# Kernel tuning notes

Hardware: AMD Instinct MI355X
Metric: run time of the kernel (lower is better)

The kernel has to match this reference:

```python
import jax, jax.numpy as jnp
import numpy as np
import math


def l2norm(x, axis):
    n = jnp.linalg.norm(x, axis=axis, keepdims=True)
    return x / jnp.maximum(n, 1e-12)


def token_pooling(x, w1, b1, w2, b2, p, w3, b3, w4, b4, eps=1e-6):
    # x: [B, L, dim_in]
    h = jnp.maximum(x @ w1 + b1, 0.0) @ w2 + b2        # [B, L, 512]
    h = l2norm(h, -1)
    # GeM over token dim L (avg_pool1d over full length == mean)
    g = jnp.mean(jnp.clip(h, eps, None) ** p, axis=1) ** (1.0 / p)  # [B, 512]
    o = jnp.maximum(g @ w3 + b3, 0.0) @ w4 + b4        # [B, dim_out]
    return l2norm(o, -1)


def sinkhorn_log(S_aug, log_a, log_b, num_iters=3):
    # S_aug: [B, m+1, n]; reg = 1.0
    M = S_aug
    u = jnp.zeros_like(log_a)
    v = jnp.zeros_like(log_b)
    def body(carry, _):
        u, v = carry
        u = log_a - jax.nn.logsumexp(M + v[:, None, :], axis=2)
        v = log_b - jax.nn.logsumexp(M + u[:, :, None], axis=1)
        return (u, v), None
    (u, v), _ = jax.lax.scan(body, (u, v), None, length=num_iters)
    return M + u[:, :, None] + v[:, None, :]


def setup_inputs() -> dict:
    key = jax.random.key(0)
    ks = jax.random.split(key, 16)
    B, S, N, C = 4, 4, 1029, 2048
    def w(k, shape):
        return jax.random.normal(k, shape, dtype=jnp.float32) * 0.02
    inp = {
        "tokens": jax.random.normal(ks[0], (B, S, N, C), dtype=jnp.float32),
        "patch_start_idx": 5,
        # camera token pooling
        "cam_w1": w(ks[1], (2048, 1024)), "cam_b1": jnp.zeros((1024,), jnp.float32),
        "cam_w2": w(ks[2], (1024, 512)),  "cam_b2": jnp.zeros((512,), jnp.float32),
        "cam_p":  jnp.ones((1,), jnp.float32) * 3.0,
        "cam_w3": w(ks[3], (512, 512)),   "cam_b3": jnp.zeros((512,), jnp.float32),
        "cam_w4": w(ks[4], (512, 256)),   "cam_b4": jnp.zeros((256,), jnp.float32),
        # register token pooling
        "reg_w1": w(ks[5], (2048, 1024)), "reg_b1": jnp.zeros((1024,), jnp.float32),
        "reg_w2": w(ks[6], (1024, 512)),  "reg_b2": jnp.zeros((512,), jnp.float32),
        "reg_p":  jnp.ones((1,), jnp.float32) * 3.0,
        "reg_w3": w(ks[7], (512, 512)),   "reg_b3": jnp.zeros((512,), jnp.float32),
        "reg_w4": w(ks[8], (512, 256)),   "reg_b4": jnp.zeros((256,), jnp.float32),
        # patch cluster features (1x1 convs == linear over channel dim)
        "pf_w1": w(ks[9], (2048, 512)),   "pf_b1": jnp.zeros((512,), jnp.float32),
        "pf_w2": w(ks[10], (512, 128)),   "pf_b2": jnp.zeros((128,), jnp.float32),
        # patch scores
        "ps_w1": w(ks[11], (2048, 512)),  "ps_b1": jnp.zeros((512,), jnp.float32),
        "ps_w2": w(ks[12], (512, 64)),    "ps_b2": jnp.zeros((64,), jnp.float32),
        "dust_bin": jnp.array(1.0, jnp.float32),
    }
    return inp


def reference(tokens, patch_start_idx, cam_w1, cam_b1, cam_w2, cam_b2, cam_p, cam_w3, cam_b3, cam_w4, cam_b4, reg_w1, reg_b1, reg_w2, reg_b2, reg_p, reg_w3, reg_b3, reg_w4, reg_b4, pf_w1, pf_b1, pf_w2, pf_b2, ps_w1, ps_b1, ps_w2, ps_b2, dust_bin):
    B, S, N, C = tokens.shape
    psi = int(patch_start_idx)
    # camera token: [B, S, C]
    camera = token_pooling(tokens[:, :, 0], cam_w1, cam_b1, cam_w2, cam_b2, cam_p, cam_w3, cam_b3, cam_w4, cam_b4)
    # register tokens: [B, S*(psi-1), C]
    reg_tok = tokens[:, :, 1:psi].reshape(B, S * (psi - 1), C)
    register = token_pooling(reg_tok, reg_w1, reg_b1, reg_w2, reg_b2, reg_p, reg_w3, reg_b3, reg_w4, reg_b4)
    # patch tokens flattened over (S, Np): n = S*Np
    patch = tokens[:, :, psi:].reshape(B, -1, C)              # [B, n, C]
    n = patch.shape[1]
    feats = jnp.maximum(patch @ pf_w1 + pf_b1, 0.0) @ pf_w2 + pf_b2   # [B, n, 128]
    scores = jnp.maximum(patch @ ps_w1 + ps_b1, 0.0) @ ps_w2 + ps_b2  # [B, n, 64]
    S_mat = jnp.swapaxes(scores, 1, 2)                        # [B, m, n]
    m = S_mat.shape[1]
    # augment with dustbin row
    dust_row = jnp.broadcast_to(dust_bin, (B, 1, n)).astype(S_mat.dtype)
    S_aug = jnp.concatenate([S_mat, dust_row], axis=1)        # [B, m+1, n]
    norm = -math.log(n + m)
    log_a = jnp.full((m + 1,), norm, dtype=S_mat.dtype).at[-1].add(math.log(n - m))
    log_b = jnp.full((n,), norm, dtype=S_mat.dtype)
    log_a = jnp.broadcast_to(log_a, (B, m + 1))
    log_b = jnp.broadcast_to(log_b, (B, n))
    log_P = sinkhorn_log(S_aug, log_a, log_b, num_iters=3) - norm
    p = jnp.exp(log_P)[:, :-1, :]                             # [B, m, n]
    # (f * p).sum(-1) as batched matmul: [B, cluster_dim, m]
    pooled = jnp.einsum('bnc,bkn->bck', feats, p)
    patch_result = l2norm(pooled, 1).reshape(B, -1)           # [B, cluster_dim*m]
    return jnp.concatenate([patch_result, camera, register], axis=-1)
```

## Files before the change

kernel.cpp:

```cpp
#include <hip/hip_runtime.h>

typedef unsigned short u16;
typedef unsigned int u32;

#define B_ 4
#define S_ 4
#define NTOK 1029
#define CDIM 2048
#define PSI 5
#define NPB 4096
#define MROWS 16384
#define N1 1024
#define N2 256
#define MD 64
#define MA 65

using bf16x8 = __attribute__((ext_vector_type(8))) short;
using f32x4  = __attribute__((ext_vector_type(4))) float;
using u16x8  = __attribute__((ext_vector_type(8))) unsigned short;

typedef __attribute__((address_space(1))) const void global_cvoid;
typedef __attribute__((address_space(3))) void lds_void;

__device__ __forceinline__ u16 f2b(float f) {
  u32 u = __builtin_bit_cast(u32, f);
  u32 r = (u + 0x7fffu + ((u >> 16) & 1u)) >> 16;
  return (u16)r;
}

__global__ void k_convert_patch(const float* __restrict__ tokens, u16* __restrict__ Abf) {
  size_t idx = (size_t)blockIdx.x * 256 + threadIdx.x;
  size_t r = idx >> 8;
  int cv = (int)(idx & 255) << 3;
  int b = (int)(r >> 12), s = (int)((r >> 10) & 3), j = (int)(r & 1023);
  const float* src = tokens + ((size_t)((b * S_ + s) * NTOK + PSI + j)) * CDIM + cv;
  float4 v0 = *(const float4*)src;
  float4 v1 = *(const float4*)(src + 4);
  u16x8 o;
  o[0] = f2b(v0.x); o[1] = f2b(v0.y); o[2] = f2b(v0.z); o[3] = f2b(v0.w);
  o[4] = f2b(v1.x); o[5] = f2b(v1.y); o[6] = f2b(v1.z); o[7] = f2b(v1.w);
  *(u16x8*)(Abf + r * CDIM + cv) = o;
}

__global__ void k_pack_patch(const float* __restrict__ pfw1, const float* __restrict__ psw1,
                             const float* __restrict__ pfw2, const float* __restrict__ psw2,
                             const float* __restrict__ pfb1, const float* __restrict__ psb1,
                             const float* __restrict__ pfb2, const float* __restrict__ psb2,
                             u16* __restrict__ W1t, u16* __restrict__ W2t,
                             float* __restrict__ b1c, float* __restrict__ b2c) {
  __shared__ float tile[32][33];
  int id = blockIdx.x, tid = threadIdx.x;
  int tx = tid & 31, ty = tid >> 5;
  if (id < 2048) {
    int kb = (id & 63) * 32, nb = (id >> 6) * 32;
    #pragma unroll
    for (int i = 0; i < 4; ++i) {
      int k = kb + ty + i * 8, n = nb + tx;
      tile[ty + i * 8][tx] = (n < 512) ? pfw1[(size_t)k * 512 + n] : psw1[(size_t)k * 512 + (n - 512)];
    }
    __syncthreads();
    #pragma unroll
    for (int i = 0; i < 4; ++i) {
      int n = nb + ty + i * 8, k = kb + tx;
      W1t[(size_t)n * CDIM + k] = f2b(tile[tx][ty + i * 8]);
    }
  } else if (id < 2304) {
    int i2 = id - 2048;
    int kb = (i2 & 31) * 32, jb = (i2 >> 5) * 32;
    #pragma unroll
    for (int i = 0; i < 4; ++i) {
      int k = kb + ty + i * 8, j = jb + tx;
      float v = 0.f;
      if (j < 128) { if (k < 512) v = pfw2[(size_t)k * 128 + j]; }
      else if (j < 192) { if (k >= 512) v = psw2[(size_t)(k - 512) * 64 + (j - 128)]; }
      tile[ty + i * 8][tx] = v;
    }
    __syncthreads();
    #pragma unroll
    for (int i = 0; i < 4; ++i) {
      int j = jb + ty + i * 8, k = kb + tx;
      W2t[(size_t)j * N1 + k] = f2b(tile[tx][ty + i * 8]);
    }
  } else {
    int t = (id - 2304) * 256 + tid;
    if (t < 1024) b1c[t] = (t < 512) ? pfb1[t] : psb1[t - 512];
    if (t < 256)  b2c[t] = (t < 128) ? pfb2[t] : ((t < 192) ? psb2[t - 128] : 0.f);
  }
}

__global__ void k_pack_cr(const float* __restrict__ camw1, const float* __restrict__ regw1,
                          const float* __restrict__ camw2, const float* __restrict__ regw2,
                          const float* __restrict__ tokens,
                          u16* __restrict__ Bt1cr, u16* __restrict__ Bt2cr,
                          u16* __restrict__ Acr) {
  __shared__ float tile[32][33];
  int id = blockIdx.x, tid = threadIdx.x;
  int tx = tid & 31, ty = tid >> 5;
  if (id < 4096) {
    const float* src = (id < 2048) ? camw1 : regw1;
    u16* dst = Bt1cr + ((id < 2048) ? 0 : (size_t)1024 * CDIM);
    int i2 = id & 2047;
    int kb = (i2 & 63) * 32, nb = (i2 >> 6) * 32;
    #pragma unroll
    for (int i = 0; i < 4; ++i)
      tile[ty + i * 8][tx] = src[(size_t)(kb + ty + i * 8) * 1024 + nb + tx];
    __syncthreads();
    #pragma unroll
    for (int i = 0; i < 4; ++i)
      dst[(size_t)(nb + ty + i * 8) * CDIM + kb + tx] = f2b(tile[tx][ty + i * 8]);
  } else if (id < 5120) {
    int i3 = id - 4096;
    const float* src = (i3 < 512) ? camw2 : regw2;
    u16* dst = Bt2cr + ((i3 < 512) ? 0 : (size_t)512 * N1);
    int i2 = i3 & 511;
    int kb = (i2 & 31) * 32, nb = (i2 >> 5) * 32;
    #pragma unroll
    for (int i = 0; i < 4; ++i)
      tile[ty + i * 8][tx] = src[(size_t)(kb + ty + i * 8) * 512 + nb + tx];
    __syncthreads();
    #pragma unroll
    for (int i = 0; i < 4; ++i)
      dst[(size_t)(nb + ty + i * 8) * N1 + kb + tx] = f2b(tile[tx][ty + i * 8]);
  } else {
    int r = id - 5120;
    int c0 = tid << 3;
    u16x8 o;
    if (r >= 80) {
      #pragma unroll
      for (int i = 0; i < 8; ++i) o[i] = 0;
    } else {
      const float* src;
      if (r < 16) { int b = r >> 2, s = r & 3; src = tokens + ((size_t)(b * S_ + s) * NTOK) * CDIM; }
      else { int r2 = r - 16; int b = r2 >> 4, q = r2 & 15, s = q >> 2, t = (q & 3) + 1;
             src = tokens + ((size_t)(b * S_ + s) * NTOK + t) * CDIM; }
      float4 v0 = *(const float4*)(src + c0);
      float4 v1 = *(const float4*)(src + c0 + 4);
      o[0] = f2b(v0.x); o[1] = f2b(v0.y); o[2] = f2b(v0.z); o[3] = f2b(v0.w);
      o[4] = f2b(v1.x); o[5] = f2b(v1.y); o[6] = f2b(v1.z); o[7] = f2b(v1.w);
    }
    *(u16x8*)(Acr + (size_t)r * CDIM + c0) = o;
  }
}

#define STAGE_TILE(buf, k0)                                                    \
  {                                                                            \
    _Pragma("unroll")                                                          \
    for (int r = 0; r < 4; ++r) {                                              \
      __builtin_amdgcn_global_load_lds(                                        \
          (global_cvoid*)(A + abase + (size_t)(r * 32) * K + (k0)),            \
          (lds_void*)(&As[buf][lofs + r * 2048]), 16, 0, 0);                   \
      __builtin_amdgcn_global_load_lds(                                        \
          (global_cvoid*)(Bt + bbase + (size_t)(r * 32) * K + (k0)),           \
          (lds_void*)(&Bs[buf][lofs + r * 2048]), 16, 0, 0);                   \
    }                                                                          \
  }

#define COMPUTE_TILE(buf)                                                      \
  {                                                                            \
    _Pragma("unroll")                                                          \
    for (int kk = 0; kk < 64; kk += 32) {                                      \
      const int csw = (kk + hi8) ^ ((lane & 7) << 3);                          \
      bf16x8 af[4], bfr[4];                                                    \
      _Pragma("unroll")                                                        \
      for (int i = 0; i < 4; ++i) {                                            \
        af[i]  = *(const bf16x8*)&As[buf][((wr << 6) + (i << 4) + (lane & 15)) * 64 + csw]; \
        bfr[i] = *(const bf16x8*)&Bs[buf][((wc << 6) + (i << 4) + (lane & 15)) * 64 + csw]; \
      }                                                                        \
      _Pragma("unroll")                                                        \
      for (int mi = 0; mi < 4; ++mi)                                           \
        _Pragma("unroll")                                                      \
        for (int ni = 0; ni < 4; ++ni)                                         \
          acc[mi][ni] = __builtin_amdgcn_mfma_f32_16x16x32_bf16(af[mi], bfr[ni], acc[mi][ni], 0, 0, 0); \
    }                                                                          \
  }

template <int RELU, int OUTBF>
__global__ __launch_bounds__(256, 2)
void k_gemm(const u16* __restrict__ A, const u16* __restrict__ Bt,
            const float* __restrict__ bias, void* __restrict__ Cout,
            int M, int N, int K) {
  __shared__ u16 As[2][128 * 64];
  __shared__ u16 Bs[2][128 * 64];
  const int tid = threadIdx.x;
  const int lane = tid & 63;
  const int wave = tid >> 6;
  const int tM = blockIdx.x << 7;
  const int tN = blockIdx.y << 7;
  const int wr = wave >> 1, wc = wave & 1;
  const int hi8 = (lane >> 4) << 3;

  const int srow = (wave << 3) + (lane >> 3);
  const int scolsw = ((lane & 7) ^ (lane >> 3)) << 3;
  const size_t abase = (size_t)(tM + srow) * K + scolsw;
  const size_t bbase = (size_t)(tN + srow) * K + scolsw;
  const int lofs = (wave << 9) + (lane << 3);

  f32x4 acc[4][4];
  #pragma unroll
  for (int i = 0; i < 4; ++i)
    #pragma unroll
    for (int j = 0; j < 4; ++j)
      acc[i][j] = (f32x4){0.f, 0.f, 0.f, 0.f};

  const int nt = K >> 6;
  STAGE_TILE(0, 0)
  STAGE_TILE(1, 64)
  for (int t = 0; t < nt; t += 2) {
    asm volatile("s_waitcnt vmcnt(8)" ::: "memory");
    __builtin_amdgcn_s_barrier();
    COMPUTE_TILE(0)
    __builtin_amdgcn_s_barrier();
    if (t + 2 < nt) STAGE_TILE(0, (t + 2) << 6)
    if (t + 1 == nt - 1) {
      asm volatile("s_waitcnt vmcnt(0)" ::: "memory");
    } else {
      asm volatile("s_waitcnt vmcnt(8)" ::: "memory");
    }
    __builtin_amdgcn_s_barrier();
    COMPUTE_TILE(1)
    __builtin_amdgcn_s_barrier();
    if (t + 3 < nt) STAGE_TILE(1, (t + 3) << 6)
  }

  #pragma unroll
  for (int ni = 0; ni < 4; ++ni) {
    const int col = tN + (wc << 6) + (ni << 4) + (lane & 15);
    const float bv = bias[col];
    #pragma unroll
    for (int mi = 0; mi < 4; ++mi) {
      #pragma unroll
      for (int j = 0; j < 4; ++j) {
        const int row = tM + (wr << 6) + (mi << 4) + ((lane >> 4) << 2) + j;
        float vv = acc[mi][ni][j] + bv;
        if (RELU) vv = fmaxf(vv, 0.f);
        if (OUTBF) ((u16*)Cout)[(size_t)row * N + col] = f2b(vv);
        else       ((float*)Cout)[(size_t)row * N + col] = vv;
      }
    }
  }
}

__global__ __launch_bounds__(256, 2)
void k_gemm_splitk(const u16* __restrict__ A, const u16* __restrict__ Bt,
                   float* __restrict__ part, int N, int K, int KC) {
  __shared__ u16 As1[128 * 64];
  __shared__ u16 Bs1[128 * 64];
  const int tid = threadIdx.x;
  const int lane = tid & 63;
  const int wave = tid >> 6;
  const int tN = blockIdx.y << 7;
  const int kb = blockIdx.z * KC;
  const int wr = wave >> 1, wc = wave & 1;
  const int srow = (wave << 3) + (lane >> 3);
  const int scol = (lane & 7) << 3;
  const size_t abase = (size_t)srow * K + scol;
  const size_t bbase = (size_t)(tN + srow) * K + scol;
  u16* asw = &As1[(wave << 9) + (lane << 3)];
  u16* bsw = &Bs1[(wave << 9) + (lane << 3)];

  f32x4 acc[4][4];
  #pragma unroll
  for (int i = 0; i < 4; ++i)
    #pragma unroll
    for (int j = 0; j < 4; ++j)
      acc[i][j] = (f32x4){0.f, 0.f, 0.f, 0.f};

  for (int k0 = kb; k0 < kb + KC; k0 += 64) {
    #pragma unroll
    for (int r = 0; r < 4; ++r) {
      __builtin_amdgcn_global_load_lds(
          (global_cvoid*)(A + abase + (size_t)(r * 32) * K + k0),
          (lds_void*)(asw + r * 2048), 16, 0, 0);
      __builtin_amdgcn_global_load_lds(
          (global_cvoid*)(Bt + bbase + (size_t)(r * 32) * K + k0),
          (lds_void*)(bsw + r * 2048), 16, 0, 0);
    }
    __syncthreads();
    #pragma unroll
    for (int kk = 0; kk < 64; kk += 32) {
      bf16x8 af[4], bfr[4];
      #pragma unroll
      for (int i = 0; i < 4; ++i) {
        af[i]  = *(const bf16x8*)&As1[((wr << 6) + (i << 4) + (lane & 15)) * 64 + kk + ((lane >> 4) << 3)];
        bfr[i] = *(const bf16x8*)&Bs1[((wc << 6) + (i << 4) + (lane & 15)) * 64 + kk + ((lane >> 4) << 3)];
      }
      #pragma unroll
      for (int mi = 0; mi < 4; ++mi)
        #pragma unroll
        for (int ni = 0; ni < 4; ++ni)
// ... 94 lines not shown
  const float* w = W3 + (size_t)(kq << 7) * 512 + o;
  #pragma unroll 8
  for (int kk = 0; kk < 128; ++kk) acc += gls[(kq << 7) + kk] * w[(size_t)kk * 512];
  part[kq][col] = acc;
  __syncthreads();
  if (kq == 0) {
    float s = part[0][col] + part[1][col] + part[2][col] + part[3][col] + B3[o];
    o1b[pb * 512 + o] = fmaxf(s, 0.f);
  }
}

__global__ __launch_bounds__(512)
void k_cr3c(const float* __restrict__ o1b,
            const float* __restrict__ camw4, const float* __restrict__ regw4,
            const float* __restrict__ camb4, const float* __restrict__ regb4,
            float* __restrict__ out) {
  __shared__ float o1s[512];
  __shared__ float part[2][256];
  __shared__ float vsq[256];
  __shared__ float red[4];
  int pb = blockIdx.x;
  bool cam = (pb < 4);
  int path = pb >> 2, b = pb & 3;
  const float* W4 = cam ? camw4 : regw4;
  const float* B4 = cam ? camb4 : regb4;
  int tid = threadIdx.x;
  o1s[tid] = o1b[pb * 512 + tid];
  __syncthreads();
  int col = tid & 255, kh = tid >> 8;
  float acc = 0.f;
  const float* w = W4 + (size_t)(kh << 8) * 256 + col;
  #pragma unroll 8
  for (int kk = 0; kk < 256; ++kk) acc += o1s[(kh << 8) + kk] * w[(size_t)kk * 256];
  part[kh][col] = acc;
  __syncthreads();
  float val = 0.f;
  if (kh == 0) {
    val = part[0][col] + part[1][col] + B4[col];
    vsq[col] = val * val;
  }
  __syncthreads();
  float ss = (tid < 256) ? vsq[tid] : 0.f;
  #pragma unroll
  for (int o = 32; o; o >>= 1) ss += __shfl_down(ss, o);
  if (tid < 256 && (tid & 63) == 0) red[tid >> 6] = ss;
  __syncthreads();
  if (kh == 0) {
    float tot = red[0] + red[1] + red[2] + red[3];
    float inv = 1.f / fmaxf(sqrtf(tot), 1e-12f);
    out[(size_t)b * 8704 + 8192 + path * 256 + col] = val * inv;
  }
}

__global__ void k_tr_scores(const float* __restrict__ FS, const float* __restrict__ dust,
                            float* __restrict__ Sc) {
  __shared__ float t[64][65];
  int b = blockIdx.x >> 6, n0 = (blockIdx.x & 63) * 64;
  int tx = threadIdx.x & 63, ty = threadIdx.x >> 6;
  for (int r = ty; r < 64; r += 4)
    t[r][tx] = FS[((size_t)(b * NPB + n0 + r)) * N2 + 128 + tx];
  __syncthreads();
  for (int k = ty; k < 64; k += 4)
    Sc[((size_t)(b * MA) + k) * NPB + n0 + tx] = t[tx][k];
  if (threadIdx.x < 64)
    Sc[((size_t)(b * MA) + 64) * NPB + n0 + threadIdx.x] = dust[0];
}

__global__ void k_sink_u(const float* __restrict__ Sc, const float* __restrict__ v,
                         float* __restrict__ u) {
  __shared__ float redm[4], reds[4];
  int b = blockIdx.x / MA, k = blockIdx.x % MA;
  const float* row = Sc + ((size_t)(b * MA) + k) * NPB;
  const float* vb = v + (size_t)b * NPB;
  int tid = threadIdx.x;
  float mx = -1e30f, s = 0.f;
  for (int n = tid; n < NPB; n += 256) {
    float x = row[n] + vb[n];
    float m2 = fmaxf(mx, x);
    s = s * __expf(mx - m2) + __expf(x - m2);
    mx = m2;
  }
  #pragma unroll
  for (int o = 32; o; o >>= 1) {
    float mo = __shfl_down(mx, o), so = __shfl_down(s, o);
    float m2 = fmaxf(mx, mo);
    s = s * __expf(mx - m2) + so * __expf(mo - m2);
    mx = m2;
  }
  if ((tid & 63) == 0) { redm[tid >> 6] = mx; reds[tid >> 6] = s; }
  __syncthreads();
  if (tid == 0) {
    float M = redm[0];
    #pragma unroll
    for (int i = 1; i < 4; ++i) M = fmaxf(M, redm[i]);
    float S = 0.f;
    #pragma unroll
    for (int i = 0; i < 4; ++i) S += reds[i] * __expf(redm[i] - M);
    const float nrm = -logf((float)(NPB + MD));
    float la = (k == MD) ? (nrm + logf((float)(NPB - MD))) : nrm;
    u[b * MA + k] = la - (M + __logf(S));
  }
}

__global__ void k_sink_v(const float* __restrict__ Sc, const float* __restrict__ u,
                         float* __restrict__ v) {
  __shared__ float us[MA];
  int b = blockIdx.x >> 4;
  int n = ((blockIdx.x & 15) << 8) + threadIdx.x;
  if (threadIdx.x < MA) us[threadIdx.x] = u[b * MA + threadIdx.x];
  __syncthreads();
  const float* Sb = Sc + (size_t)b * MA * NPB + n;
  float mx = -1e30f;
  for (int k = 0; k < MA; ++k) mx = fmaxf(mx, Sb[(size_t)k * NPB] + us[k]);
  float s = 0.f;
  for (int k = 0; k < MA; ++k) s += __expf(Sb[(size_t)k * NPB] + us[k] - mx);
  const float nrm = -logf((float)(NPB + MD));
  v[(size_t)b * NPB + n] = nrm - (mx + __logf(s));
}

__global__ __launch_bounds__(256)
void k_pooled1(const float* __restrict__ FS, const float* __restrict__ Sc,
               const float* __restrict__ u, const float* __restrict__ v,
               float* __restrict__ partial) {
  __shared__ float Fs[64][132];
  __shared__ float Ps[64][68];
  int b = blockIdx.x >> 6, j = blockIdx.x & 63;
  int n0 = j << 6;
  int tid = threadIdx.x;
  {
    int r = tid >> 5;
    int c4 = (tid & 31) << 2;
    #pragma unroll
    for (int i = 0; i < 8; ++i) {
      int n = r + (i << 3);
      float4 vv = *(const float4*)&FS[((size_t)(b * NPB + n0 + n)) * N2 + c4];
      *(float4*)&Fs[n][c4] = vv;
    }
  }
  {
    const float nrm = -logf((float)(NPB + MD));
    int r = tid >> 4;
    int c4 = (tid & 15) << 2;
    #pragma unroll
    for (int i = 0; i < 4; ++i) {
      int k = r + (i << 4);
      float uk = u[b * MA + k];
      float4 sv = *(const float4*)&Sc[((size_t)(b * MA) + k) * NPB + n0 + c4];
      float4 vv = *(const float4*)&v[(size_t)b * NPB + n0 + c4];
      float4 o;
      o.x = __expf(sv.x + uk + vv.x - nrm);
      o.y = __expf(sv.y + uk + vv.y - nrm);
      o.z = __expf(sv.z + uk + vv.z - nrm);
      o.w = __expf(sv.w + uk + vv.w - nrm);
      *(float4*)&Ps[k][c4] = o;
    }
  }
  __syncthreads();
  int tc = tid & 31, tk = tid >> 5;
  int c0 = tc << 2, k0 = tk << 3;
  float acc[4][8];
  #pragma unroll
  for (int i = 0; i < 4; ++i)
    #pragma unroll
    for (int kk = 0; kk < 8; ++kk) acc[i][kk] = 0.f;
  for (int n = 0; n < 64; ++n) {
    float4 f = *(const float4*)&Fs[n][c0];
    float pv[8];
    #pragma unroll
    for (int kk = 0; kk < 8; ++kk) pv[kk] = Ps[k0 + kk][n];
    #pragma unroll
    for (int i = 0; i < 4; ++i) {
      float fv = ((const float*)&f)[i];
      #pragma unroll
      for (int kk = 0; kk < 8; ++kk) acc[i][kk] += fv * pv[kk];
    }
  }
  float* dst = partial + ((size_t)(b * 64 + j) << 13);
  #pragma unroll
  for (int i = 0; i < 4; ++i) {
    float4 lo = {acc[i][0], acc[i][1], acc[i][2], acc[i][3]};
    float4 hi = {acc[i][4], acc[i][5], acc[i][6], acc[i][7]};
    *(float4*)&dst[((c0 + i) << 6) + k0] = lo;
    *(float4*)&dst[((c0 + i) << 6) + k0 + 4] = hi;
  }
}

__global__ void k_pooled2(const float* __restrict__ partial, float* __restrict__ pooled) {
  int o = blockIdx.x * 256 + threadIdx.x;
  int b = o >> 13, rem = o & 8191;
  const float* src = partial + ((size_t)b << 19) + rem;
  float s = 0.f;
  #pragma unroll 8
  for (int j = 0; j < 64; ++j) s += src[(size_t)j << 13];
  pooled[o] = s;
}

__global__ void k_patch_out(const float* __restrict__ pooled, float* __restrict__ out) {
  int b = blockIdx.x >> 6, k = blockIdx.x & 63;
  int tid = threadIdx.x;
  float v0 = pooled[((size_t)(b * 128) + tid) * MD + k];
  float v1 = pooled[((size_t)(b * 128) + 64 + tid) * MD + k];
  float ss = v0 * v0 + v1 * v1;
  #pragma unroll
  for (int o = 32; o; o >>= 1) ss += __shfl_down(ss, o);
  ss = __shfl(ss, 0);
  float inv = 1.f / fmaxf(sqrtf(ss), 1e-12f);
  out[(size_t)b * 8704 + tid * 64 + k] = v0 * inv;
  out[(size_t)b * 8704 + (64 + tid) * 64 + k] = v1 * inv;
}

#define OFF_ABF 0u
#define OFF_SC 0u
#define OFF_U 4259840u
#define OFF_V 4263936u
#define OFF_POOL 8523776u
#define OFF_HP 8982528u
#define OFF_H 67108864u
#define OFF_PART OFF_H
#define OFF_CP1 75497472u
#define OFF_GSB OFF_CP1
#define OFF_O1B 75513856u
#define OFF_CP2 83886080u
#define OFF_BT1CR 88080384u
#define OFF_BT2CR 96468992u
#define OFF_ACR 98566144u
#define OFF_A2 99090432u
#define OFF_FS 100663296u
#define OFF_W1T 117440512u
#define OFF_W2T 121634816u
#define OFF_B1C 122159104u
#define OFF_B2C 122163200u

extern "C" void kernel_launch(void* const* d_in, const int* in_sizes, int n_in,
                              void* d_out, int out_size, void* d_ws, size_t ws_size,
                              hipStream_t stream) {
  (void)in_sizes; (void)n_in; (void)out_size; (void)ws_size;
  const float* tokens = (const float*)d_in[0];
  const float* cam_w1 = (const float*)d_in[2];
  const float* cam_b1 = (const float*)d_in[3];
  const float* cam_w2 = (const float*)d_in[4];
  const float* cam_b2 = (const float*)d_in[5];
  const float* cam_p  = (const float*)d_in[6];
  const float* cam_w3 = (const float*)d_in[7];
  const float* cam_b3 = (const float*)d_in[8];
  const float* cam_w4 = (const float*)d_in[9];
  const float* cam_b4 = (const float*)d_in[10];
  const float* reg_w1 = (const float*)d_in[11];
  const float* reg_b1 = (const float*)d_in[12];
  const float* reg_w2 = (const float*)d_in[13];
  const float* reg_b2 = (const float*)d_in[14];
  const float* reg_p  = (const float*)d_in[15];
  const float* reg_w3 = (const float*)d_in[16];
  const float* reg_b3 = (const float*)d_in[17];
  const float* reg_w4 = (const float*)d_in[18];
  const float* reg_b4 = (const float*)d_in[19];
  const float* pf_w1  = (const float*)d_in[20];
  const float* pf_b1  = (const float*)d_in[21];
  const float* pf_w2  = (const float*)d_in[22];
  const float* pf_b2  = (const float*)d_in[23];
  const float* ps_w1  = (const float*)d_in[24];
  const float* ps_b1  = (const float*)d_in[25];
  const float* ps_w2  = (const float*)d_in[26];
  const float* ps_b2  = (const float*)d_in[27];
  const float* dust   = (const float*)d_in[28];
  float* out = (float*)d_out;
  char* ws = (char*)d_ws;

  u16* Abf = (u16*)(ws + OFF_ABF);
  float* Sc = (float*)(ws + OFF_SC);
  float* ub = (float*)(ws + OFF_U);
  float* vb = (float*)(ws + OFF_V);
  float* pooled = (float*)(ws + OFF_POOL);
  float* hp = (float*)(ws + OFF_HP);
  u16* H   = (u16*)(ws + OFF_H);
  float* partial = (float*)(ws + OFF_PART);
  float* cp1 = (float*)(ws + OFF_CP1);
  float* gsb = (float*)(ws + OFF_GSB);
  float* o1b = (float*)(ws + OFF_O1B);
  float* cp2 = (float*)(ws + OFF_CP2);
  u16* Bt1cr = (u16*)(ws + OFF_BT1CR);
  u16* Bt2cr = (u16*)(ws + OFF_BT2CR);
  u16* Acr = (u16*)(ws + OFF_ACR);
  u16* A2  = (u16*)(ws + OFF_A2);
  float* FS = (float*)(ws + OFF_FS);
  u16* W1t = (u16*)(ws + OFF_W1T);
  u16* W2t = (u16*)(ws + OFF_W2T);
  float* b1c = (float*)(ws + OFF_B1C);
  float* b2c = (float*)(ws + OFF_B2C);

  hipMemsetAsync(vb, 0, (size_t)B_ * NPB * sizeof(float), stream);

  k_convert_patch<<<16384, 256, 0, stream>>>(tokens, Abf);
  k_pack_patch<<<2308, 256, 0, stream>>>(pf_w1, ps_w1, pf_w2, ps_w2,
                                         pf_b1, ps_b1, pf_b2, ps_b2,
                                         W1t, W2t, b1c, b2c);
  k_gemm<1, 1><<<dim3(128, 8), 256, 0, stream>>>(Abf, W1t, b1c, (void*)H, MROWS, N1, CDIM);
  k_gemm<0, 0><<<dim3(128, 2), 256, 0, stream>>>(H, W2t, b2c, (void*)FS, MROWS, N2, N1);

  k_pack_cr<<<5248, 256, 0, stream>>>(cam_w1, reg_w1, cam_w2, reg_w2, tokens,
                                      Bt1cr, Bt2cr, Acr);
  k_gemm_splitk<<<dim3(1, 16, 8), 256, 0, stream>>>(Acr, Bt1cr, cp1, 2048, CDIM, 256);
  k_cr_fin1<<<dim3(128, 4), 256, 0, stream>>>(cp1, cam_b1, reg_b1, A2);
  k_gemm_splitk<<<dim3(1, 8, 8), 256, 0, stream>>>(A2, Bt2cr, cp2, 1024, N1, 128);
  k_cr_fin2<<<80, 512, 0, stream>>>(cp2, cam_b2, reg_b2, cam_p, reg_p, hp);
  k_cr3a<<<8, 512, 0, stream>>>(hp, cam_p, reg_p, gsb);
  k_cr3b<<<dim3(8, 4), 512, 0, stream>>>(gsb, cam_w3, reg_w3, cam_b3, reg_b3, o1b);
  k_cr3c<<<8, 512, 0, stream>>>(o1b, cam_w4, reg_w4, cam_b4, reg_b4, out);

  k_tr_scores<<<256, 256, 0, stream>>>(FS, dust, Sc);
  for (int it = 0; it < 3; ++it) {
    k_sink_u<<<B_ * MA, 256, 0, stream>>>(Sc, vb, ub);
    k_sink_v<<<B_ * 16, 256, 0, stream>>>(Sc, ub, vb);
  }
  k_pooled1<<<B_ * 64, 256, 0, stream>>>(FS, Sc, ub, vb, partial);
  k_pooled2<<<128, 256, 0, stream>>>(partial, pooled);
  k_patch_out<<<B_ * MD, 64, 0, stream>>>(pooled, out);
}
```

Baseline: 244.3 us.

## Use 256x256-tile 512-thread GEMM for the first patch MLP layer

Adds a new bf16 MFMA GEMM kernel with 256x256 output tiles, 8 waves per block, double-buffered LDS staging through global_load_lds, and an XOR swizzle. It replaces the 128x128 GEMM for the big first layer (16384x1024x2048). Larger tiles raise arithmetic intensity and cut redundant global loads. The cost is 256 blocks on a 256-CU device, a single block per CU (launch bounds 1), 128KB of LDS, and high register pressure from the 8x4 accumulators.

Measured after the change: 242.6 us. No clear change (-0.7%).

```diff
diff --git a/kernel.cpp b/kernel.cpp
--- a/kernel.cpp
+++ b/kernel.cpp
@@ -139,6 +139,107 @@
       o[4] = f2b(v1.x); o[5] = f2b(v1.y); o[6] = f2b(v1.z); o[7] = f2b(v1.w);
     }
     *(u16x8*)(Acr + (size_t)r * CDIM + c0) = o;
+  }
+}
+
+#define STAGE_TILE256(buf, k0)                                                 \
+  {                                                                            \
+    _Pragma("unroll")                                                          \
+    for (int r = 0; r < 4; ++r) {                                              \
+      __builtin_amdgcn_global_load_lds(                                        \
+          (global_cvoid*)(A + abase + (size_t)(r * 64) * K + (k0)),            \
+          (lds_void*)(&As[buf][(r << 12) + lofs]), 16, 0, 0);                  \
+      __builtin_amdgcn_global_load_lds(                                        \
+          (global_cvoid*)(Bt + bbase + (size_t)(r * 64) * K + (k0)),           \
+          (lds_void*)(&Bs[buf][(r << 12) + lofs]), 16, 0, 0);                  \
+    }                                                                          \
+  }
+
+#define COMPUTE_TILE256(buf)                                                   \
+  {                                                                            \
+    _Pragma("unroll")                                                          \
+    for (int kk = 0; kk < 64; kk += 32) {                                      \
+      const int csw = (kk + hi8) ^ ((lane & 7) << 3);                          \
+      bf16x8 bfr[4], af[8];                                                    \
+      _Pragma("unroll")                                                        \
+      for (int i = 0; i < 4; ++i)                                              \
+        bfr[i] = *(const bf16x8*)&Bs[buf][((wc << 6) + (i << 4) + (lane & 15)) * 64 + csw]; \
+      _Pragma("unroll")                                                        \
+      for (int i = 0; i < 8; ++i)                                              \
+        af[i]  = *(const bf16x8*)&As[buf][((wr << 7) + (i << 4) + (lane & 15)) * 64 + csw]; \
+      __builtin_amdgcn_s_setprio(1);                                           \
+      _Pragma("unroll")                                                        \
+      for (int mi = 0; mi < 8; ++mi)                                           \
+        _Pragma("unroll")                                                      \
+        for (int ni = 0; ni < 4; ++ni)                                         \
+          acc[mi][ni] = __builtin_amdgcn_mfma_f32_16x16x32_bf16(af[mi], bfr[ni], acc[mi][ni], 0, 0, 0); \
+      __builtin_amdgcn_s_setprio(0);                                           \
+    }                                                                          \
+  }
+
+template <int RELU, int OUTBF>
+__global__ __launch_bounds__(512, 1)
+void k_gemm256(const u16* __restrict__ A, const u16* __restrict__ Bt,
+               const float* __restrict__ bias, void* __restrict__ Cout,
+               int M, int N, int K) {
+  __shared__ u16 As[2][256 * 64];
+  __shared__ u16 Bs[2][256 * 64];
+  const int tid = threadIdx.x;
+  const int lane = tid & 63;
+  const int wave = tid >> 6;
+  const int tM = blockIdx.x << 8;
+  const int tN = blockIdx.y << 8;
+  const int wr = wave >> 2, wc = wave & 3;
+  const int hi8 = (lane >> 4) << 3;
+
+  const int srow = tid >> 3;
+  const int scolsw = ((tid & 7) ^ (srow & 7)) << 3;
+  const size_t abase = (size_t)(tM + srow) * K + scolsw;
+  const size_t bbase = (size_t)(tN + srow) * K + scolsw;
+  const int lofs = tid << 3;
+
+  f32x4 acc[8][4];
+  #pragma unroll
+  for (int i = 0; i < 8; ++i)
+    #pragma unroll
+    for (int j = 0; j < 4; ++j)
+      acc[i][j] = (f32x4){0.f, 0.f, 0.f, 0.f};
+
+  const int nt = K >> 6;
+  STAGE_TILE256(0, 0)
+  STAGE_TILE256(1, 64)
+  for (int t = 0; t < nt; t += 2) {
+    asm volatile("s_waitcnt vmcnt(8)" ::: "memory");
+    __builtin_amdgcn_s_barrier();
+    COMPUTE_TILE256(0)
+    __builtin_amdgcn_s_barrier();
+    if (t + 2 < nt) STAGE_TILE256(0, (t + 2) << 6)
+    if (t + 1 == nt - 1) {
+      asm volatile("s_waitcnt vmcnt(0)" ::: "memory");
+    } else {
+      asm volatile("s_waitcnt vmcnt(8)" ::: "memory");
+    }
+    __builtin_amdgcn_s_barrier();
+    COMPUTE_TILE256(1)
+    __builtin_amdgcn_s_barrier();
+    if (t + 3 < nt) STAGE_TILE256(1, (t + 3) << 6)
+  }
+
+  #pragma unroll
+  for (int ni = 0; ni < 4; ++ni) {
+    const int col = tN + (wc << 6) + (ni << 4) + (lane & 15);
+    const float bv = bias[col];
+    #pragma unroll
+    for (int mi = 0; mi < 8; ++mi) {
+      #pragma unroll
+      for (int j = 0; j < 4; ++j) {
+        const int row = tM + (wr << 7) + (mi << 4) + ((lane >> 4) << 2) + j;
+        float vv = acc[mi][ni][j] + bv;
+        if (RELU) vv = fmaxf(vv, 0.f);
+        if (OUTBF) ((u16*)Cout)[(size_t)row * N + col] = f2b(vv);
+        else       ((float*)Cout)[(size_t)row * N + col] = vv;
+      }
+    }
   }
 }
 
@@ -677,7 +778,7 @@
   k_pack_patch<<<2308, 256, 0, stream>>>(pf_w1, ps_w1, pf_w2, ps_w2,
                                          pf_b1, ps_b1, pf_b2, ps_b2,
                                          W1t, W2t, b1c, b2c);
-  k_gemm<1, 1><<<dim3(128, 8), 256, 0, stream>>>(Abf, W1t, b1c, (void*)H, MROWS, N1, CDIM);
+  k_gemm256<1, 1><<<dim3(64, 4), 512, 0, stream>>>(Abf, W1t, b1c, (void*)H, MROWS, N1, CDIM);
   k_gemm<0, 0><<<dim3(128, 2), 256, 0, stream>>>(H, W2t, b2c, (void*)FS, MROWS, N2, N1);
 
   k_pack_cr<<<5248, 256, 0, stream>>>(cam_w1, reg_w1, cam_w2, reg_w2, tokens,
```

## Fuse fp32-to-bf16 conversion into first GEMM and merge Sinkhorn into one kernel

Applied to the files above, without the earlier changes.

The separate conversion pass that turned patch tokens into a bf16 buffer is removed. The first patch GEMM now loads fp32 tokens into registers, converts them, and writes them into swizzled LDS, overlapping those loads with MFMA compute, so the 64MB bf16 intermediate is never written or read back. The score transpose and the three Sinkhorn u/v iterations are merged into one persistent 256-block kernel that uses an atomic grid barrier, replacing seven small launches. The risks are more register pressure in the GEMM and a possible deadlock if the 256 blocks are not all resident at once.

After: 530.7 us. +117.2%, slower.

```diff
diff --git a/kernel.cpp b/kernel.cpp
--- a/kernel.cpp
+++ b/kernel.cpp
@@ -26,20 +26,6 @@
   u32 u = __builtin_bit_cast(u32, f);
   u32 r = (u + 0x7fffu + ((u >> 16) & 1u)) >> 16;
   return (u16)r;
-}
-
-__global__ void k_convert_patch(const float* __restrict__ tokens, u16* __restrict__ Abf) {
-  size_t idx = (size_t)blockIdx.x * 256 + threadIdx.x;
-  size_t r = idx >> 8;
-  int cv = (int)(idx & 255) << 3;
-  int b = (int)(r >> 12), s = (int)((r >> 10) & 3), j = (int)(r & 1023);
-  const float* src = tokens + ((size_t)((b * S_ + s) * NTOK + PSI + j)) * CDIM + cv;
-  float4 v0 = *(const float4*)src;
-  float4 v1 = *(const float4*)(src + 4);
-  u16x8 o;
-  o[0] = f2b(v0.x); o[1] = f2b(v0.y); o[2] = f2b(v0.z); o[3] = f2b(v0.w);
-  o[4] = f2b(v1.x); o[5] = f2b(v1.y); o[6] = f2b(v1.z); o[7] = f2b(v1.w);
-  *(u16x8*)(Abf + r * CDIM + cv) = o;
 }
 
 __global__ void k_pack_patch(const float* __restrict__ pfw1, const float* __restrict__ psw1,
@@ -142,19 +128,6 @@
   }
 }
 
-#define STAGE_TILE(buf, k0)                                                    \
-  {                                                                            \
-    _Pragma("unroll")                                                          \
-    for (int r = 0; r < 4; ++r) {                                              \
-      __builtin_amdgcn_global_load_lds(                                        \
-          (global_cvoid*)(A + abase + (size_t)(r * 32) * K + (k0)),            \
-          (lds_void*)(&As[buf][lofs + r * 2048]), 16, 0, 0);                   \
-      __builtin_amdgcn_global_load_lds(                                        \
-          (global_cvoid*)(Bt + bbase + (size_t)(r * 32) * K + (k0)),           \
-          (lds_void*)(&Bs[buf][lofs + r * 2048]), 16, 0, 0);                   \
-    }                                                                          \
-  }
-
 #define COMPUTE_TILE(buf)                                                      \
   {                                                                            \
     _Pragma("unroll")                                                          \
@@ -174,6 +147,109 @@
     }                                                                          \
   }
 
+#define LOADA(regs, k0)                                                        \
+  { _Pragma("unroll") for (int q = 0; q < 8; ++q)                              \
+      regs[q] = *(const float4*)(asrc + (k0) + (q << 2)); }
+
+#define WRITEA(buf, regs)                                                      \
+  { _Pragma("unroll") for (int g = 0; g < 4; ++g) {                            \
+      u16x8 w; float4 x = regs[2 * g], y = regs[2 * g + 1];                    \
+      w[0] = f2b(x.x); w[1] = f2b(x.y); w[2] = f2b(x.z); w[3] = f2b(x.w);      \
+      w[4] = f2b(y.x); w[5] = f2b(y.y); w[6] = f2b(y.z); w[7] = f2b(y.w);      \
+      *(u16x8*)&As[buf][awofs + ((achalf + (g << 3)) ^ aswz)] = w; } }
+
+#define BSTAGE(buf, k0)                                                        \
+  { _Pragma("unroll") for (int r = 0; r < 4; ++r)                              \
+      __builtin_amdgcn_global_load_lds(                                        \
+          (global_cvoid*)(Bt + bbase + (size_t)(r * 32) * CDIM + (k0)),        \
+          (lds_void*)(&Bs[buf][lofs + r * 2048]), 16, 0, 0); }
+
+__global__ __launch_bounds__(256, 2)
+void k_gemm1f(const float* __restrict__ tokens, const u16* __restrict__ Bt,
+              const float* __restrict__ bias, u16* __restrict__ Cout) {
+  __shared__ u16 As[2][128 * 64];
+  __shared__ u16 Bs[2][128 * 64];
+  const int tid = threadIdx.x;
+  const int lane = tid & 63;
+  const int wave = tid >> 6;
+  const int tM = blockIdx.x << 7;
+  const int tN = blockIdx.y << 7;
+  const int wr = wave >> 1, wc = wave & 1;
+  const int hi8 = (lane >> 4) << 3;
+
+  const int arow = tid >> 1;
+  const int achalf = (tid & 1) << 5;
+  const int panel = blockIdx.x >> 3;
+  const int j0 = (blockIdx.x & 7) << 7;
+  const float* asrc = tokens + ((size_t)(panel * NTOK + PSI + j0 + arow)) * CDIM + achalf;
+  const int awofs = arow << 6;
+  const int aswz = (arow & 7) << 3;
+
+  const int srow = (wave << 3) + (lane >> 3);
+  const int scolsw = ((lane & 7) ^ (lane >> 3)) << 3;
+  const size_t bbase = (size_t)(tN + srow) * CDIM + scolsw;
+  const int lofs = (wave << 9) + (lane << 3);
+
+  f32x4 acc[4][4];
+  #pragma unroll
+  for (int i = 0; i < 4; ++i)
+    #pragma unroll
+    for (int j = 0; j < 4; ++j)
+      acc[i][j] = (f32x4){0.f, 0.f, 0.f, 0.f};
+
+  float4 a0[8], a1[8];
+  LOADA(a0, 0) WRITEA(0, a0)
+  LOADA(a1, 64) WRITEA(1, a1)
+  BSTAGE(0, 0) BSTAGE(1, 64)
+  const int nt = CDIM >> 6;
+  for (int t = 0; t < nt; t += 2) {
+    if (t + 2 < nt) LOADA(a0, (t + 2) << 6)
+    asm volatile("s_waitcnt vmcnt(12) lgkmcnt(0)" ::: "memory");
+    __builtin_amdgcn_s_barrier();
+    COMPUTE_TILE(0)
+    __builtin_amdgcn_s_barrier();
+    if (t + 2 < nt) { WRITEA(0, a0) BSTAGE(0, (t + 2) << 6) }
+    if (t + 3 < nt) LOADA(a1, (t + 3) << 6)
+    if (t + 1 == nt - 1) {
+      asm volatile("s_waitcnt vmcnt(0) lgkmcnt(0)" ::: "memory");
+    } else {
+      asm volatile("s_waitcnt vmcnt(12) lgkmcnt(0)" ::: "memory");
+    }
+    __builtin_amdgcn_s_barrier();
+    COMPUTE_TILE(1)
+    __builtin_amdgcn_s_barrier();
+    if (t + 3 < nt) { WRITEA(1, a1) BSTAGE(1, (t + 3) << 6) }
+  }
+
+  #pragma unroll
+  for (int ni = 0; ni < 4; ++ni) {
+    const int col = tN + (wc << 6) + (ni << 4) + (lane & 15);
+    const float bv = bias[col];
+    #pragma unroll
+    for (int mi = 0; mi < 4; ++mi) {
+      #pragma unroll
+      for (int j = 0; j < 4; ++j) {
+        const int row = tM + (wr << 6) + (mi << 4) + ((lane >> 4) << 2) + j;
+        float vv = fmaxf(acc[mi][ni][j] + bv, 0.f);
+        Cout[(size_t)row * N1 + col] = f2b(vv);
+      }
+    }
+  }
+}
+
+#define STAGE_TILE(buf, k0)                                                    \
+  {                                                                            \
+    _Pragma("unroll")                                                          \
+    for (int r = 0; r < 4; ++r) {                                              \
+      __builtin_amdgcn_global_load_lds(                                        \
+          (global_cvoid*)(A + abase + (size_t)(r * 32) * K + (k0)),            \
+          (lds_void*)(&As[buf][lofs + r * 2048]), 16, 0, 0);                   \
+      __builtin_amdgcn_global_load_lds(                                        \
+          (global_cvoid*)(Bt + bbase + (size_t)(r * 32) * K + (k0)),           \
+          (lds_void*)(&Bs[buf][lofs + r * 2048]), 16, 0, 0);                   \
+    }                                                                          \
+  }
+
 template <int RELU, int OUTBF>
 __global__ __launch_bounds__(256, 2)
 void k_gemm(const u16* __restrict__ A, const u16* __restrict__ Bt,
@@ -435,70 +511,91 @@
   }
 }
 
-__global__ void k_tr_scores(const float* __restrict__ FS, const float* __restrict__ dust,
-                            float* __restrict__ Sc) {
-  __shared__ float t[64][65];
-  int b = blockIdx.x >> 6, n0 = (blockIdx.x & 63) * 64;
-  int tx = threadIdx.x & 63, ty = threadIdx.x >> 6;
-  for (int r = ty; r < 64; r += 4)
-    t[r][tx] = FS[((size_t)(b * NPB + n0 + r)) * N2 + 128 + tx];
-  __syncthreads();
-  for (int k = ty; k < 64; k += 4)
-    Sc[((size_t)(b * MA) + k) * NPB + n0 + tx] = t[tx][k];
-  if (threadIdx.x < 64)
-    Sc[((size_t)(b * MA) + 64) * NPB + n0 + threadIdx.x] = dust[0];
-}
-
-__global__ void k_sink_u(const float* __restrict__ Sc, const float* __restrict__ v,
-                         float* __restrict__ u) {
+__device__ __forceinline__ void gridbar(u32* cnt, u32 target) {
+  __syncthreads();
+  if (threadIdx.x == 0) {
+    __threadfence();
+    __hip_atomic_fetch_add(cnt, 1u, __ATOMIC_ACQ_REL, __HIP_MEMORY_SCOPE_AGENT);
+    while (__hip_atomic_load(cnt, __ATOMIC_ACQUIRE, __HIP_MEMORY_SCOPE_AGENT) < target) {}
+  }
+  __syncthreads();
+  __threadfence();
+}
+
+__global__ __launch_bounds__(256)
+void k_sink_fused(const float* __restrict__ FS, const float* __restrict__ dust,
+                  float* __restrict__ Sc, float* __restrict__ u, float* __restrict__ v,
+                  u32* __restrict__ bar) {
+  __shared__ float t64[64][65];
   __shared__ float redm[4], reds[4];
-  int b = blockIdx.x / MA, k = blockIdx.x % MA;
-  const float* row = Sc + ((size_t)(b * MA) + k) * NPB;
-  const float* vb = v + (size_t)b * NPB;
-  int tid = threadIdx.x;
-  float mx = -1e30f, s = 0.f;
-  for (int n = tid; n < NPB; n += 256) {
-    float x = row[n] + vb[n];
-    float m2 = fmaxf(mx, x);
-    s = s * __expf(mx - m2) + __expf(x - m2);
-    mx = m2;
-  }
-  #pragma unroll
-  for (int o = 32; o; o >>= 1) {
-    float mo = __shfl_down(mx, o), so = __shfl_down(s, o);
-    float m2 = fmaxf(mx, mo);
-    s = s * __expf(mx - m2) + so * __expf(mo - m2);
-    mx = m2;
-  }
-  if ((tid & 63) == 0) { redm[tid >> 6] = mx; reds[tid >> 6] = s; }
-  __syncthreads();
-  if (tid == 0) {
-    float M = redm[0];
-    #pragma unroll
-    for (int i = 1; i < 4; ++i) M = fmaxf(M, redm[i]);
-    float S = 0.f;
-    #pragma unroll
-    for (int i = 0; i < 4; ++i) S += reds[i] * __expf(redm[i] - M);
-    const float nrm = -logf((float)(NPB + MD));
-    float la = (k == MD) ? (nrm + logf((float)(NPB - MD))) : nrm;
-    u[b * MA + k] = la - (M + __logf(S));
-  }
-}
-
-__global__ void k_sink_v(const float* __restrict__ Sc, const float* __restrict__ u,
-                         float* __restrict__ v) {
   __shared__ float us[MA];
-  int b = blockIdx.x >> 4;
-  int n = ((blockIdx.x & 15) << 8) + threadIdx.x;
-  if (threadIdx.x < MA) us[threadIdx.x] = u[b * MA + threadIdx.x];
-  __syncthreads();
-  const float* Sb = Sc + (size_t)b * MA * NPB + n;
-  float mx = -1e30f;
-  for (int k = 0; k < MA; ++k) mx = fmaxf(mx, Sb[(size_t)k * NPB] + us[k]);
-  float s = 0.f;
-  for (int k = 0; k < MA; ++k) s += __expf(Sb[(size_t)k * NPB] + us[k] - mx);
+  const int tid = threadIdx.x, bid = blockIdx.x;
   const float nrm = -logf((float)(NPB + MD));
-  v[(size_t)b * NPB + n] = nrm - (mx + __logf(s));
+  u32 tgt = 256;
+
+  {
+    int b = bid >> 6, n0 = (bid & 63) * 64;
+    int tx = tid & 63, ty = tid >> 6;
+    for (int r = ty; r < 64; r += 4)
+      t64[r][tx] = FS[((size_t)(b * NPB + n0 + r)) * N2 + 128 + tx];
+    __syncthreads();
+    for (int k = ty; k < 64; k += 4)
+      Sc[((size_t)(b * MA) + k) * NPB + n0 + tx] = t64[tx][k];
+    if (tid < 64)
+      Sc[((size_t)(b * MA) + 64) * NPB + n0 + tid] = dust[0];
+    if (bid < 64) v[bid * 256 + tid] = 0.f;
+  }
+  gridbar(bar, tgt); tgt += 256;
+
+  for (int it = 0; it < 3; ++it) {
+    for (int row = bid; row < B_ * MA; row += 256) {
+      int b = row / MA, k = row % MA;
+      const float* rp = Sc + ((size_t)(b * MA) + k) * NPB;
+      const float* vp = v + (size_t)b * NPB;
+      float mx = -1e30f, s = 0.f;
+      for (int n = tid; n < NPB; n += 256) {
+        float x = rp[n] + vp[n];
+        float m2 = fmaxf(mx, x);
+        s = s * __expf(mx - m2) + __expf(x - m2);
+        mx = m2;
+      }
+      #pragma unroll
+      for (int o = 32; o; o >>= 1) {
+        float mo = __shfl_down(mx, o), so = __shfl_down(s, o);
+        float m2 = fmaxf(mx, mo);
+        s = s * __expf(mx - m2) + so * __expf(mo - m2);
+        mx = m2;
+      }
+      if ((tid & 63) == 0) { redm[tid >> 6] = mx; reds[tid >> 6] = s; }
+      __syncthreads();
+      if (tid == 0) {
+        float M = redm[0];
+        #pragma unroll
+        for (int i = 1; i < 4; ++i) M = fmaxf(M, redm[i]);
+        float S = 0.f;
+        #pragma unroll
+        for (int i = 0; i < 4; ++i) S += reds[i] * __expf(redm[i] - M);
+        float la = (k == MD) ? (nrm + logf((float)(NPB - MD))) : nrm;
+        u[b * MA + k] = la - (M + __logf(S));
+      }
+      __syncthreads();
+    }
+    gridbar(bar, tgt); tgt += 256;
+
+    if (bid < 64) {
+      int b = bid >> 4;
+      int n = ((bid & 15) << 8) + tid;
+      if (tid < MA) us[tid] = u[b * MA + tid];
+      __syncthreads();
+      const float* Sb = Sc + (size_t)b * MA * NPB + n;
+      float mx = -1e30f;
+      for (int k = 0; k < MA; ++k) mx = fmaxf(mx, Sb[(size_t)k * NPB] + us[k]);
+      float s = 0.f;
+      for (int k = 0; k < MA; ++k) s += __expf(Sb[(size_t)k * NPB] + us[k] - mx);
+      v[(size_t)b * NPB + n] = nrm - (mx + __logf(s));
+    }
+    if (it < 2) { gridbar(bar, tgt); tgt += 256; }
+  }
 }
 
 __global__ __launch_bounds__(256)
@@ -592,7 +689,6 @@
   out[(size_t)b * 8704 + (64 + tid) * 64 + k] = v1 * inv;
 }
 
-#define OFF_ABF 0u
 #define OFF_SC 0u
 #define OFF_U 4259840u
 #define OFF_V 4263936u
@@ -613,6 +709,7 @@
 #define OFF_W2T 121634816u
 #define OFF_B1C 122159104u
 #define OFF_B2C 122163200u
+#define OFF_GBAR 122164224u
 
 extern "C" void kernel_launch(void* const* d_in, const int* in_sizes, int n_in,
                               void* d_out, int out_size, void* d_ws, size_t ws_size,
@@ -649,7 +746,6 @@
   float* out = (float*)d_out;
   char* ws = (char*)d_ws;
 
-  u16* Abf = (u16*)(ws + OFF_ABF);
   float* Sc = (float*)(ws + OFF_SC);
   float* ub = (float*)(ws + OFF_U);
   float* vb = (float*)(ws + OFF_V);
@@ -670,14 +766,14 @@
   u16* W2t = (u16*)(ws + OFF_W2T);
   float* b1c = (float*)(ws + OFF_B1C);
   float* b2c = (float*)(ws + OFF_B2C);
-
-  hipMemsetAsync(vb, 0, (size_t)B_ * NPB * sizeof(float), stream);
-
-  k_convert_patch<<<16384, 256, 0, stream>>>(tokens, Abf);
+  u32* gbar = (u32*)(ws + OFF_GBAR);
+
+  hipMemsetAsync(gbar, 0, 64, stream);
+
   k_pack_patch<<<2308, 256, 0, stream>>>(pf_w1, ps_w1, pf_w2, ps_w2,
                                          pf_b1, ps_b1, pf_b2, ps_b2,
                                          W1t, W2t, b1c, b2c);
-  k_gemm<1, 1><<<dim3(128, 8), 256, 0, stream>>>(Abf, W1t, b1c, (void*)H, MROWS, N1, CDIM);
+  k_gemm1f<<<dim3(128, 8), 256, 0, stream>>>(tokens, W1t, b1c, H);
   k_gemm<0, 0><<<dim3(128, 2), 256, 0, stream>>>(H, W2t, b2c, (void*)FS, MROWS, N2, N1);
 
   k_pack_cr<<<5248, 256, 0, stream>>>(cam_w1, reg_w1, cam_w2, reg_w2, tokens,
@@ -690,11 +786,7 @@
   k_cr3b<<<dim3(8, 4), 512, 0, stream>>>(gsb, cam_w3, reg_w3, cam_b3, reg_b3, o1b);
   k_cr3c<<<8, 512, 0, stream>>>(o1b, cam_w4, reg_w4, cam_b4, reg_b4, out);
 
-  k_tr_scores<<<256, 256, 0, stream>>>(FS, dust, Sc);
-  for (int it = 0; it < 3; ++it) {
-    k_sink_u<<<B_ * MA, 256, 0, stream>>>(Sc, vb, ub);
-    k_sink_v<<<B_ * 16, 256, 0, stream>>>(Sc, ub, vb);
-  }
+  k_sink_fused<<<256, 256, 0, stream>>>(FS, dust, Sc, ub, vb, gbar);
   k_pooled1<<<B_ * 64, 256, 0, stream>>>(FS, Sc, ub, vb, partial);
   k_pooled2<<<128, 256, 0, stream>>>(partial, pooled);
   k_patch_out<<<B_ * MD, 64, 0, stream>>>(pooled, out);
```

## Fuse patch prep kernels and write transposed scores from GEMM epilogue

Applied to the files above, without the earlier changes.

Merges the token bf16 conversion and patch weight packing into one launch. The second patch GEMM's epilogue now also writes the score columns transposed into the Sinkhorn score buffer, which removes the separate transpose kernel. The dustbin row is no longer stored; the Sinkhorn kernels read the dust scalar directly. This saves two launches and a read/write pass over the scores. The cost is scattered, poorly coalesced stores in the GEMM epilogue.

New measurement: 243.1 us (median of 2 runs). No clear change (-0.5%).

```diff
diff --git a/kernel.cpp b/kernel.cpp
--- a/kernel.cpp
+++ b/kernel.cpp
@@ -28,21 +28,8 @@
   return (u16)r;
 }
 
-__global__ void k_convert_patch(const float* __restrict__ tokens, u16* __restrict__ Abf) {
-  size_t idx = (size_t)blockIdx.x * 256 + threadIdx.x;
-  size_t r = idx >> 8;
-  int cv = (int)(idx & 255) << 3;
-  int b = (int)(r >> 12), s = (int)((r >> 10) & 3), j = (int)(r & 1023);
-  const float* src = tokens + ((size_t)((b * S_ + s) * NTOK + PSI + j)) * CDIM + cv;
-  float4 v0 = *(const float4*)src;
-  float4 v1 = *(const float4*)(src + 4);
-  u16x8 o;
-  o[0] = f2b(v0.x); o[1] = f2b(v0.y); o[2] = f2b(v0.z); o[3] = f2b(v0.w);
-  o[4] = f2b(v1.x); o[5] = f2b(v1.y); o[6] = f2b(v1.z); o[7] = f2b(v1.w);
-  *(u16x8*)(Abf + r * CDIM + cv) = o;
-}
-
-__global__ void k_pack_patch(const float* __restrict__ pfw1, const float* __restrict__ psw1,
+__global__ void k_prep_patch(const float* __restrict__ tokens, u16* __restrict__ Abf,
+                             const float* __restrict__ pfw1, const float* __restrict__ psw1,
                              const float* __restrict__ pfw2, const float* __restrict__ psw2,
                              const float* __restrict__ pfb1, const float* __restrict__ psb1,
                              const float* __restrict__ pfb2, const float* __restrict__ psb2,
@@ -50,9 +37,24 @@
                              float* __restrict__ b1c, float* __restrict__ b2c) {
   __shared__ float tile[32][33];
   int id = blockIdx.x, tid = threadIdx.x;
+  if (id < 16384) {
+    size_t idx = (size_t)id * 256 + tid;
+    size_t r = idx >> 8;
+    int cv = (int)(idx & 255) << 3;
+    int b = (int)(r >> 12), s = (int)((r >> 10) & 3), j = (int)(r & 1023);
+    const float* src = tokens + ((size_t)((b * S_ + s) * NTOK + PSI + j)) * CDIM + cv;
+    float4 v0 = *(const float4*)src;
+    float4 v1 = *(const float4*)(src + 4);
+    u16x8 o;
+    o[0] = f2b(v0.x); o[1] = f2b(v0.y); o[2] = f2b(v0.z); o[3] = f2b(v0.w);
+    o[4] = f2b(v1.x); o[5] = f2b(v1.y); o[6] = f2b(v1.z); o[7] = f2b(v1.w);
+    *(u16x8*)(Abf + r * CDIM + cv) = o;
+    return;
+  }
+  int id2 = id - 16384;
   int tx = tid & 31, ty = tid >> 5;
-  if (id < 2048) {
-    int kb = (id & 63) * 32, nb = (id >> 6) * 32;
+  if (id2 < 2048) {
+    int kb = (id2 & 63) * 32, nb = (id2 >> 6) * 32;
     #pragma unroll
     for (int i = 0; i < 4; ++i) {
       int k = kb + ty + i * 8, n = nb + tx;
@@ -64,8 +66,8 @@
       int n = nb + ty + i * 8, k = kb + tx;
       W1t[(size_t)n * CDIM + k] = f2b(tile[tx][ty + i * 8]);
     }
-  } else if (id < 2304) {
-    int i2 = id - 2048;
+  } else if (id2 < 2304) {
+    int i2 = id2 - 2048;
     int kb = (i2 & 31) * 32, jb = (i2 >> 5) * 32;
     #pragma unroll
     for (int i = 0; i < 4; ++i) {
@@ -82,7 +84,7 @@
       W2t[(size_t)j * N1 + k] = f2b(tile[tx][ty + i * 8]);
     }
   } else {
-    int t = (id - 2304) * 256 + tid;
+    int t = (id2 - 2304) * 256 + tid;
     if (t < 1024) b1c[t] = (t < 512) ? pfb1[t] : psb1[t - 512];
     if (t < 256)  b2c[t] = (t < 128) ? pfb2[t] : ((t < 192) ? psb2[t - 128] : 0.f);
   }
@@ -174,11 +176,11 @@
     }                                                                          \
   }
 
-template <int RELU, int OUTBF>
+template <int RELU, int OUTBF, int WRSC>
 __global__ __launch_bounds__(256, 2)
 void k_gemm(const u16* __restrict__ A, const u16* __restrict__ Bt,
             const float* __restrict__ bias, void* __restrict__ Cout,
-            int M, int N, int K) {
+            int M, int N, int K, float* __restrict__ ScOut) {
   __shared__ u16 As[2][128 * 64];
   __shared__ u16 Bs[2][128 * 64];
   const int tid = threadIdx.x;
@@ -235,6 +237,10 @@
         if (RELU) vv = fmaxf(vv, 0.f);
         if (OUTBF) ((u16*)Cout)[(size_t)row * N + col] = f2b(vv);
         else       ((float*)Cout)[(size_t)row * N + col] = vv;
+        if (WRSC) {
+          if (col >= 128 && col < 192)
+            ScOut[((size_t)((row >> 12) * MD + (col - 128))) * NPB + (row & 4095)] = vv;
+        }
       }
     }
   }
@@ -435,33 +441,29 @@
   }
 }
 
-__global__ void k_tr_scores(const float* __restrict__ FS, const float* __restrict__ dust,
-                            float* __restrict__ Sc) {
-  __shared__ float t[64][65];
-  int b = blockIdx.x >> 6, n0 = (blockIdx.x & 63) * 64;
-  int tx = threadIdx.x & 63, ty = threadIdx.x >> 6;
-  for (int r = ty; r < 64; r += 4)
-    t[r][tx] = FS[((size_t)(b * NPB + n0 + r)) * N2 + 128 + tx];
-  __syncthreads();
-  for (int k = ty; k < 64; k += 4)
-    Sc[((size_t)(b * MA) + k) * NPB + n0 + tx] = t[tx][k];
-  if (threadIdx.x < 64)
-    Sc[((size_t)(b * MA) + 64) * NPB + n0 + threadIdx.x] = dust[0];
-}
-
 __global__ void k_sink_u(const float* __restrict__ Sc, const float* __restrict__ v,
-                         float* __restrict__ u) {
+                         float* __restrict__ u, const float* __restrict__ dust) {
   __shared__ float redm[4], reds[4];
   int b = blockIdx.x / MA, k = blockIdx.x % MA;
-  const float* row = Sc + ((size_t)(b * MA) + k) * NPB;
   const float* vb = v + (size_t)b * NPB;
   int tid = threadIdx.x;
   float mx = -1e30f, s = 0.f;
-  for (int n = tid; n < NPB; n += 256) {
-    float x = row[n] + vb[n];
-    float m2 = fmaxf(mx, x);
-    s = s * __expf(mx - m2) + __expf(x - m2);
-    mx = m2;
+  if (k < MD) {
+    const float* row = Sc + ((size_t)(b * MD) + k) * NPB;
+    for (int n = tid; n < NPB; n += 256) {
+      float x = row[n] + vb[n];
+      float m2 = fmaxf(mx, x);
+      s = s * __expf(mx - m2) + __expf(x - m2);
+      mx = m2;
+    }
+  } else {
+    float d0 = dust[0];
+    for (int n = tid; n < NPB; n += 256) {
+      float x = d0 + vb[n];
+      float m2 = fmaxf(mx, x);
+      s = s * __expf(mx - m2) + __expf(x - m2);
+      mx = m2;
+    }
   }
   #pragma unroll
   for (int o = 32; o; o >>= 1) {
@@ -486,17 +488,18 @@
 }
 
 __global__ void k_sink_v(const float* __restrict__ Sc, const float* __restrict__ u,
-                         float* __restrict__ v) {
+                         float* __restrict__ v, const float* __restrict__ dust) {
   __shared__ float us[MA];
   int b = blockIdx.x >> 4;
   int n = ((blockIdx.x & 15) << 8) + threadIdx.x;
   if (threadIdx.x < MA) us[threadIdx.x] = u[b * MA + threadIdx.x];
   __syncthreads();
-  const float* Sb = Sc + (size_t)b * MA * NPB + n;
-  float mx = -1e30f;
-  for (int k = 0; k < MA; ++k) mx = fmaxf(mx, Sb[(size_t)k * NPB] + us[k]);
-  float s = 0.f;
-  for (int k = 0; k < MA; ++k) s += __expf(Sb[(size_t)k * NPB] + us[k] - mx);
+  const float* Sb = Sc + (size_t)b * MD * NPB + n;
+  float d0 = dust[0];
+  float mx = d0 + us[MD];
+  for (int k = 0; k < MD; ++k) mx = fmaxf(mx, Sb[(size_t)k * NPB] + us[k]);
+  float s = __expf(d0 + us[MD] - mx);
+  for (int k = 0; k < MD; ++k) s += __expf(Sb[(size_t)k * NPB] + us[k] - mx);
   const float nrm = -logf((float)(NPB + MD));
   v[(size_t)b * NPB + n] = nrm - (mx + __logf(s));
 }
@@ -528,7 +531,7 @@
     for (int i = 0; i < 4; ++i) {
       int k = r + (i << 4);
       float uk = u[b * MA + k];
-      float4 sv = *(const float4*)&Sc[((size_t)(b * MA) + k) * NPB + n0 + c4];
+      float4 sv = *(const float4*)&Sc[((size_t)(b * MD) + k) * NPB + n0 + c4];
       float4 vv = *(const float4*)&v[(size_t)b * NPB + n0 + c4];
       float4 o;
       o.x = __expf(sv.x + uk + vv.x - nrm);
@@ -673,12 +676,13 @@
 
   hipMemsetAsync(vb, 0, (size_t)B_ * NPB * sizeof(float), stream);
 
-  k_convert_patch<<<16384, 256, 0, stream>>>(tokens, Abf);
-  k_pack_patch<<<2308, 256, 0, stream>>>(pf_w1, ps_w1, pf_w2, ps_w2,
-                                         pf_b1, ps_b1, pf_b2, ps_b2,
-                                         W1t, W2t, b1c, b2c);
-  k_gemm<1, 1><<<dim3(128, 8), 256, 0, stream>>>(Abf, W1t, b1c, (void*)H, MROWS, N1, CDIM);
-  k_gemm<0, 0><<<dim3(128, 2), 256, 0, stream>>>(H, W2t, b2c, (void*)FS, MROWS, N2, N1);
+  k_prep_patch<<<18692, 256, 0, stream>>>(tokens, Abf, pf_w1, ps_w1, pf_w2, ps_w2,
+                                          pf_b1, ps_b1, pf_b2, ps_b2,
+                                          W1t, W2t, b1c, b2c);
+  k_gemm<1, 1, 0><<<dim3(128, 8), 256, 0, stream>>>(Abf, W1t, b1c, (void*)H,
+                                                    MROWS, N1, CDIM, nullptr);
+  k_gemm<0, 0, 1><<<dim3(128, 2), 256, 0, stream>>>(H, W2t, b2c, (void*)FS,
+                                                    MROWS, N2, N1, Sc);
 
   k_pack_cr<<<5248, 256, 0, stream>>>(cam_w1, reg_w1, cam_w2, reg_w2, tokens,
                                       Bt1cr, Bt2cr, Acr);
@@ -690,10 +694,9 @@
   k_cr3b<<<dim3(8, 4), 512, 0, stream>>>(gsb, cam_w3, reg_w3, cam_b3, reg_b3, o1b);
   k_cr3c<<<8, 512, 0, stream>>>(o1b, cam_w4, reg_w4, cam_b4, reg_b4, out);
 
-  k_tr_scores<<<256, 256, 0, stream>>>(FS, dust, Sc);
   for (int it = 0; it < 3; ++it) {
-    k_sink_u<<<B_ * MA, 256, 0, stream>>>(Sc, vb, ub);
-    k_sink_v<<<B_ * 16, 256, 0, stream>>>(Sc, ub, vb);
+    k_sink_u<<<B_ * MA, 256, 0, stream>>>(Sc, vb, ub, dust);
+    k_sink_v<<<B_ * 16, 256, 0, stream>>>(Sc, ub, vb, dust);
   }
   k_pooled1<<<B_ * 64, 256, 0, stream>>>(FS, Sc, ub, vb, partial);
   k_pooled2<<<128, 256, 0, stream>>>(partial, pooled);
```
